# Kernel tuning notes

Measured on AMD Instinct MI355X. Metric: run time of the kernel, lower is better.

The kernel has to match this reference:

```python
import jax, jax.numpy as jnp
import numpy as np

CUT_SIZE = 224
CUTN = 128
SIDE = 1024
CUT_POW = 1.0


def setup_inputs() -> dict:
    key = jax.random.key(0)
    x = jax.random.uniform(key, (1, 3, SIDE, SIDE), dtype=jnp.float32)
    rng = np.random.default_rng(0)
    max_size = SIDE
    min_size = min(SIDE, SIDE, CUT_SIZE)
    r = rng.random(CUTN)
    sizes = (r ** CUT_POW * (max_size - min_size) + min_size).astype(np.int32)
    oy = np.array([rng.integers(0, SIDE - int(s) + 1) for s in sizes], dtype=np.int32)
    ox = np.array([rng.integers(0, SIDE - int(s) + 1) for s in sizes], dtype=np.int32)
    return {
        "input": x,
        "sizes": jnp.asarray(sizes),
        "offsety": jnp.asarray(oy),
        "offsetx": jnp.asarray(ox),
    }


def _cutout(img, size, oy, ox):
    # img: [B, C, H, W]; crop a size x size window at (oy, ox) and bilinearly
    # resample to CUT_SIZE x CUT_SIZE (align_corners=False convention).
    H, W = img.shape[2], img.shape[3]
    scale = size.astype(jnp.float32) / CUT_SIZE
    coords = (jnp.arange(CUT_SIZE, dtype=jnp.float32) + 0.5) * scale - 0.5
    ys = jnp.clip(oy.astype(jnp.float32) + coords, 0.0, H - 1.0)
    xs = jnp.clip(ox.astype(jnp.float32) + coords, 0.0, W - 1.0)
    y0 = jnp.floor(ys).astype(jnp.int32)
    x0 = jnp.floor(xs).astype(jnp.int32)
    y1 = jnp.minimum(y0 + 1, H - 1)
    x1 = jnp.minimum(x0 + 1, W - 1)
    wy = (ys - y0.astype(jnp.float32))[None, None, :, None]
    wx = (xs - x0.astype(jnp.float32))[None, None, None, :]
    # separable bilinear: interpolate rows, then columns
    rows = img[:, :, y0, :] * (1.0 - wy) + img[:, :, y1, :] * wy  # [B,C,cs,W]
    out = rows[:, :, :, x0] * (1.0 - wx) + rows[:, :, :, x1] * wx  # [B,C,cs,cs]
    return out


def _make_cutouts(input, sizes, offsety, offsetx):
    cuts = jax.vmap(_cutout, in_axes=(None, 0, 0, 0))(input, sizes, offsety, offsetx)
    # [cutn, B, C, cs, cs] -> torch.cat(dim=0) layout [cutn*B, C, cs, cs]
    n, b, c, h, w = cuts.shape
    return cuts.reshape(n * b, c, h, w)


def reference(input, sizes, offsety, offsetx):
    out = _make_cutouts(input, sizes, offsety, offsetx)
    # ClampWithGrad forward is a plain clamp
    return jnp.clip(out, 0.0, 1.0)
```

## Files before the change

### kernel.cpp

```cpp
#include <hip/hip_runtime.h>
#include <hip/hip_fp16.h>

#define CUT_SIZE 224
#define SIDE 1024
#define CUTN 128
#define NSLAB 8
#define SLAB_BLOCKS 192
#define SLAB_WSLOTS (SLAB_BLOCKS * 4)
#define LDSW2 1032

__global__ __launch_bounds__(256) void cutout_fused_kernel(
    const float* __restrict__ img,
    const int* __restrict__ sizes,
    const int* __restrict__ offy,
    const int* __restrict__ offx,
    float* __restrict__ out)
{
    __shared__ __half lds[4][3][LDSW2];
    const int s    = blockIdx.x & 7;
    const int w    = threadIdx.x >> 6;
    const int lane = threadIdx.x & 63;
    const int t    = threadIdx.x;
    const unsigned q = (unsigned)(blockIdx.x >> 3) * 4u + (unsigned)w;

    float* pf  = reinterpret_cast<float*>(&lds[0][0][0]);
    int*   pi  = reinterpret_cast<int*>(&lds[0][0][0]);
    float* fInv = pf;
    float* fOy  = pf + 128;
    int*   iWt  = pi + 256;
    int*   cdf  = pi + 384;
    int*   qbv  = pi + 513;
    int*   lenv = pi + 522;
    int*   rlov = pi + 650;
    int*   scv  = pi + 778;

    if (t < CUTN) {
        const int sz = sizes[t];
        fInv[t] = (float)CUT_SIZE / (float)sz;
        fOy[t]  = (float)offy[t];
        iWt[t]  = 100 + (sz >> 2);
    }
    __syncthreads();

    if (t <= 128) {
        const float Yf = (float)(t << 3);
        int c = 0;
        for (int n = 0; n < CUTN; ++n) {
            const float thr = (Yf + 0.5f - fOy[n]) * fInv[n] - 0.5f;
            c += min(CUT_SIZE, max(0, (int)ceilf(thr))) * iWt[n];
        }
        cdf[t] = c;
    }
    __syncthreads();

    if (t >= 1 && t < NSLAB) {
        const long long target = (long long)t * (long long)cdf[128] / NSLAB;
        int lo = 0, hi = 128;
        while (hi - lo > 1) { const int m = (lo + hi) >> 1;
                              if ((long long)cdf[m] >= target) hi = m; else lo = m; }
        qbv[t] = hi << 3;
    }
    if (t == 0) { qbv[0] = 0; qbv[NSLAB] = SIDE; }
    __syncthreads();

    if (t < CUTN) {
        int rlo, rhi;
        { const int Y = qbv[s];
          rlo = (Y <= 0) ? 0
              : min(CUT_SIZE, max(0, (int)ceilf(((float)Y + 0.5f - fOy[t]) * fInv[t] - 0.5f))); }
        { const int Y = qbv[s + 1];
          rhi = (Y >= SIDE) ? CUT_SIZE
              : min(CUT_SIZE, max(0, (int)ceilf(((float)Y + 0.5f - fOy[t]) * fInv[t] - 0.5f))); }
        rlov[t] = rlo;
        lenv[t] = rhi - rlo;
        scv[t]  = rhi - rlo;
    }
    __syncthreads();
    for (int off = 1; off < CUTN; off <<= 1) {
        int v = 0;
        if (t < CUTN && t >= off) v = scv[t - off];
        __syncthreads();
        if (t < CUTN) scv[t] += v;
        __syncthreads();
    }

    const unsigned aLo = (unsigned)(scv[lane]      - lenv[lane]);
    const unsigned aHi = (unsigned)(scv[64 + lane] - lenv[64 + lane]);
    const unsigned bLo = (unsigned)rlov[lane];
    const unsigned bHi = (unsigned)rlov[64 + lane];
    const unsigned T   = (unsigned)scv[CUTN - 1];
    const float   szLo = (float)sizes[lane], szHi = (float)sizes[64 + lane];
    const float   oyLo = (float)offy[lane],  oyHi = (float)offy[64 + lane];
    const float   oxLo = (float)offx[lane],  oxHi = (float)offx[64 + lane];
    __syncthreads();

    __half* __restrict__ l0 = &lds[w][0][0];
    __half* __restrict__ l1 = &lds[w][1][0];
    __half* __restrict__ l2 = &lds[w][2][0];

    for (unsigned i = q; i < T; i += SLAB_WSLOTS) {
        int n = 0;
        unsigned An = 0;
#pragma unroll
        for (int st = 64; st; st >>= 1) {
            const int m = n | st;
            const unsigned Am = (m & 64) ? (unsigned)__shfl((int)aHi, m & 63)
                                         : (unsigned)__shfl((int)aLo, m & 63);
            if (Am <= i) { n = m; An = Am; }
        }
        const int hi6 = n & 64, lo6 = n & 63;
        const unsigned rlo = hi6 ? (unsigned)__shfl((int)bHi, lo6)
                                 : (unsigned)__shfl((int)bLo, lo6);
        const int   y  = (int)rlo + (int)(i - An);
        const float sz = hi6 ? __shfl(szHi, lo6) : __shfl(szLo, lo6);
        const float oy = hi6 ? __shfl(oyHi, lo6) : __shfl(oyLo, lo6);
        const float ox = hi6 ? __shfl(oxHi, lo6) : __shfl(oxLo, lo6);

        const float scale = sz * (1.0f / (float)CUT_SIZE);

        float fy = fmaf((float)y + 0.5f, scale, oy - 0.5f);
        fy = fminf(fmaxf(fy, 0.0f), (float)(SIDE - 1));
        const int   y0 = (int)fy;
        const int   y1 = min(y0 + 1, SIDE - 1);
        const float wy  = fy - (float)y0;
        const float wy0 = 1.0f - wy;

        float fx0 = fmaf(0.5f, scale, ox - 0.5f);
        fx0 = fminf(fmaxf(fx0, 0.0f), (float)(SIDE - 1));
        float fxl = fmaf((float)CUT_SIZE - 0.5f, scale, ox - 0.5f);
        fxl = fminf(fmaxf(fxl, 0.0f), (float)(SIDE - 1));
        const int xb    = (int)fx0;
        const int xe    = min((int)fxl + 1, SIDE - 1);
        const int xb4   = xb & ~3;
        const int ilast = xe - xb4;
        const int nf4   = (ilast >> 2) + 1;

        const size_t cstride = (size_t)SIDE * SIDE;
        const float* b0 = img + (size_t)y0 * SIDE + xb4;
        const float* b1 = img + (size_t)y1 * SIDE + xb4;
        const float4* __restrict__ rp0 = reinterpret_cast<const float4*>(b0);
        const float4* __restrict__ rq0 = reinterpret_cast<const float4*>(b1);
        const float4* __restrict__ rp1 = reinterpret_cast<const float4*>(b0 + cstride);
        const float4* __restrict__ rq1 = reinterpret_cast<const float4*>(b1 + cstride);
        const float4* __restrict__ rp2 = reinterpret_cast<const float4*>(b0 + 2 * cstride);
        const float4* __restrict__ rq2 = reinterpret_cast<const float4*>(b1 + 2 * cstride);

        for (int k = lane; k < nf4; k += 64) {
            const float4 a0 = rp0[k], c0 = rq0[k];
            const float4 a1 = rp1[k], c1 = rq1[k];
            const float4 a2 = rp2[k], c2 = rq2[k];
            union { __half2 h[2]; uint2 u; } pk;
            pk.h[0] = __floats2half2_rn(a0.x * wy0 + c0.x * wy, a0.y * wy0 + c0.y * wy);
            pk.h[1] = __floats2half2_rn(a0.z * wy0 + c0.z * wy, a0.w * wy0 + c0.w * wy);
            *reinterpret_cast<uint2*>(l0 + 4 * k) = pk.u;
            pk.h[0] = __floats2half2_rn(a1.x * wy0 + c1.x * wy, a1.y * wy0 + c1.y * wy);
            pk.h[1] = __floats2half2_rn(a1.z * wy0 + c1.z * wy, a1.w * wy0 + c1.w * wy);
            *reinterpret_cast<uint2*>(l1 + 4 * k) = pk.u;
            pk.h[0] = __floats2half2_rn(a2.x * wy0 + c2.x * wy, a2.y * wy0 + c2.y * wy);
            pk.h[1] = __floats2half2_rn(a2.z * wy0 + c2.z * wy, a2.w * wy0 + c2.w * wy);
            *reinterpret_cast<uint2*>(l2 + 4 * k) = pk.u;
        }
        if (lane < 3) (&lds[w][lane][0])[ilast + 1] = __float2half(0.0f);
        asm volatile("s_waitcnt lgkmcnt(0)" ::: "memory");

        const int p0 = lane << 2;
        if (p0 < CUT_SIZE) {
            const float xb4f = (float)xb4;
            float fx = fmaf((float)p0 + 0.5f, scale, ox - 0.5f);
            float4 o0, o1, o2;
            float* v0 = &o0.x; float* v1 = &o1.x; float* v2 = &o2.x;
#pragma unroll
            for (int j = 0; j < 4; ++j) {
                const float fxj = fminf(fmaxf(fx, 0.0f), (float)(SIDE - 1));
                fx += scale;
                const float fl = fxj - xb4f;
                const int   i0 = (int)fl;
                const float wx  = fl - (float)i0;
                const float wx0 = 1.0f - wx;
                v0[j] = fminf(fmaxf(__half2float(l0[i0]) * wx0 + __half2float(l0[i0 + 1]) * wx, 0.0f), 1.0f);
                v1[j] = fminf(fmaxf(__half2float(l1[i0]) * wx0 + __half2float(l1[i0 + 1]) * wx, 0.0f), 1.0f);
                v2[j] = fminf(fmaxf(__half2float(l2[i0]) * wx0 + __half2float(l2[i0 + 1]) * wx, 0.0f), 1.0f);
            }
            const size_t obase = (((size_t)n * 3) * CUT_SIZE + y) * CUT_SIZE + p0;
            *reinterpret_cast<float4*>(out + obase) = o0;
            *reinterpret_cast<float4*>(out + obase + CUT_SIZE * CUT_SIZE) = o1;
            *reinterpret_cast<float4*>(out + obase + 2 * (CUT_SIZE * CUT_SIZE)) = o2;
        }
        asm volatile("" ::: "memory");
    }
}

extern "C" void kernel_launch(void* const* d_in, const int* in_sizes, int n_in,
                              void* d_out, int out_size, void* d_ws, size_t ws_size,
                              hipStream_t stream) {
    const float* img   = (const float*)d_in[0];
    const int*   sizes = (const int*)d_in[1];
    const int*   offy  = (const int*)d_in[2];
    const int*   offx  = (const int*)d_in[3];
    float*       out   = (float*)d_out;

    cutout_fused_kernel<<<NSLAB * SLAB_BLOCKS, 256, 0, stream>>>(
        img, sizes, offy, offx, out);
}
```

Baseline: 38.53 us.

## Stream source rows into LDS via global_load_lds DMA with column-chunked tasks

Replaces the per-lane float4 loads and fp16 vertical pre-interpolation with direct global-to-LDS DMA (global_load_lds, 16 bytes per lane) of fixed 256-float windows for both source rows of all three channels. Each output row is split into column chunks so the source span fits the window, and the work balancing is changed to count chunk tasks. Interpolation now runs entirely in fp32 from LDS, which also removes the half-precision rounding. The cost is more tasks with redundant window loads, scalar instead of float4 output stores, and a full vmcnt wait with no overlap between loading and compute.

```diff
diff --git a/kernel.cpp b/kernel.cpp
--- a/kernel.cpp
+++ b/kernel.cpp
@@ -1,5 +1,4 @@
 #include <hip/hip_runtime.h>
-#include <hip/hip_fp16.h>
 
 #define CUT_SIZE 224
 #define SIDE 1024
@@ -7,38 +6,50 @@
 #define NSLAB 8
 #define SLAB_BLOCKS 192
 #define SLAB_WSLOTS (SLAB_BLOCKS * 4)
-#define LDSW2 1032
-
-__global__ __launch_bounds__(256) void cutout_fused_kernel(
+#define WINF 256
+#define LWAVE (6 * WINF + 8)
+
+__device__ __forceinline__ void dma16(const float* g, float* l) {
+    __builtin_amdgcn_global_load_lds(
+        (const __attribute__((address_space(1))) void*)g,
+        (__attribute__((address_space(3))) void*)l, 16, 0, 0);
+}
+
+__global__ __launch_bounds__(256) void cutout_dma_kernel(
     const float* __restrict__ img,
     const int* __restrict__ sizes,
     const int* __restrict__ offy,
     const int* __restrict__ offx,
     float* __restrict__ out)
 {
-    __shared__ __half lds[4][3][LDSW2];
+    __shared__ float lds[4][LWAVE];
     const int s    = blockIdx.x & 7;
     const int w    = threadIdx.x >> 6;
     const int lane = threadIdx.x & 63;
     const int t    = threadIdx.x;
     const unsigned q = (unsigned)(blockIdx.x >> 3) * 4u + (unsigned)w;
 
-    float* pf  = reinterpret_cast<float*>(&lds[0][0][0]);
-    int*   pi  = reinterpret_cast<int*>(&lds[0][0][0]);
+    float* pf   = &lds[0][0];
+    int*   pi   = reinterpret_cast<int*>(&lds[0][0]);
     float* fInv = pf;
     float* fOy  = pf + 128;
-    int*   iWt  = pi + 256;
-    int*   cdf  = pi + 384;
-    int*   qbv  = pi + 513;
-    int*   lenv = pi + 522;
-    int*   rlov = pi + 650;
-    int*   scv  = pi + 778;
+    int*   iWN  = pi + 256;
+    int*   iWt  = pi + 384;
+    int*   cdf  = pi + 512;
+    int*   qbv  = pi + 641;
+    int*   lenv = pi + 650;
+    int*   rlov = pi + 778;
+    int*   scv  = pi + 906;
 
     if (t < CUTN) {
         const int sz = sizes[t];
         fInv[t] = (float)CUT_SIZE / (float)sz;
         fOy[t]  = (float)offy[t];
-        iWt[t]  = 100 + (sz >> 2);
+        int wout = 55552 / sz;
+        if (wout > CUT_SIZE) wout = CUT_SIZE;
+        const int nch = (CUT_SIZE + wout - 1) / wout;
+        iWN[t] = wout | (nch << 16);
+        iWt[t] = 8 + 5 * nch;
     }
     __syncthreads();
 
@@ -72,8 +83,9 @@
           rhi = (Y >= SIDE) ? CUT_SIZE
               : min(CUT_SIZE, max(0, (int)ceilf(((float)Y + 0.5f - fOy[t]) * fInv[t] - 0.5f))); }
         rlov[t] = rlo;
-        lenv[t] = rhi - rlo;
-        scv[t]  = rhi - rlo;
+        const int tasks = (rhi - rlo) * (iWN[t] >> 16);
+        lenv[t] = tasks;
+        scv[t]  = tasks;
     }
     __syncthreads();
     for (int off = 1; off < CUTN; off <<= 1) {
@@ -86,17 +98,16 @@
 
     const unsigned aLo = (unsigned)(scv[lane]      - lenv[lane]);
     const unsigned aHi = (unsigned)(scv[64 + lane] - lenv[64 + lane]);
-    const unsigned bLo = (unsigned)rlov[lane];
-    const unsigned bHi = (unsigned)rlov[64 + lane];
+    const unsigned rLo = (unsigned)rlov[lane],      rHi = (unsigned)rlov[64 + lane];
+    const unsigned wnLo = (unsigned)iWN[lane],      wnHi = (unsigned)iWN[64 + lane];
     const unsigned T   = (unsigned)scv[CUTN - 1];
     const float   szLo = (float)sizes[lane], szHi = (float)sizes[64 + lane];
     const float   oyLo = (float)offy[lane],  oyHi = (float)offy[64 + lane];
     const float   oxLo = (float)offx[lane],  oxHi = (float)offx[64 + lane];
     __syncthreads();
 
-    __half* __restrict__ l0 = &lds[w][0][0];
-    __half* __restrict__ l1 = &lds[w][1][0];
-    __half* __restrict__ l2 = &lds[w][2][0];
+    float* __restrict__ lw = &lds[w][0];
+    const size_t cs = (size_t)SIDE * SIDE;
 
     for (unsigned i = q; i < T; i += SLAB_WSLOTS) {
         int n = 0;
@@ -109,12 +120,21 @@
             if (Am <= i) { n = m; An = Am; }
         }
         const int hi6 = n & 64, lo6 = n & 63;
-        const unsigned rlo = hi6 ? (unsigned)__shfl((int)bHi, lo6)
-                                 : (unsigned)__shfl((int)bLo, lo6);
-        const int   y  = (int)rlo + (int)(i - An);
+        const unsigned rlo = hi6 ? (unsigned)__shfl((int)rHi, lo6)
+                                 : (unsigned)__shfl((int)rLo, lo6);
+        const unsigned wnc = hi6 ? (unsigned)__shfl((int)wnHi, lo6)
+                                 : (unsigned)__shfl((int)wnLo, lo6);
         const float sz = hi6 ? __shfl(szHi, lo6) : __shfl(szLo, lo6);
         const float oy = hi6 ? __shfl(oyHi, lo6) : __shfl(oyLo, lo6);
         const float ox = hi6 ? __shfl(oxHi, lo6) : __shfl(oxLo, lo6);
+        const int wout = (int)(wnc & 0xffffu);
+        const int nch  = (int)(wnc >> 16);
+
+        const unsigned rem = i - An;
+        const float nchinv = __builtin_amdgcn_rcpf((float)nch);
+        const int row_off = (int)(((float)rem + 0.5f) * nchinv);
+        const int chunk   = (int)rem - row_off * nch;
+        const int y       = (int)rlo + row_off;
 
         const float scale = sz * (1.0f / (float)CUT_SIZE);
 
@@ -125,66 +145,45 @@
         const float wy  = fy - (float)y0;
         const float wy0 = 1.0f - wy;
 
-        float fx0 = fmaf(0.5f, scale, ox - 0.5f);
-        fx0 = fminf(fmaxf(fx0, 0.0f), (float)(SIDE - 1));
-        float fxl = fmaf((float)CUT_SIZE - 0.5f, scale, ox - 0.5f);
-        fxl = fminf(fmaxf(fxl, 0.0f), (float)(SIDE - 1));
-        const int xb    = (int)fx0;
-        const int xe    = min((int)fxl + 1, SIDE - 1);
-        const int xb4   = xb & ~3;
-        const int ilast = xe - xb4;
-        const int nf4   = (ilast >> 2) + 1;
-
-        const size_t cstride = (size_t)SIDE * SIDE;
-        const float* b0 = img + (size_t)y0 * SIDE + xb4;
-        const float* b1 = img + (size_t)y1 * SIDE + xb4;
-        const float4* __restrict__ rp0 = reinterpret_cast<const float4*>(b0);
-        const float4* __restrict__ rq0 = reinterpret_cast<const float4*>(b1);
-        const float4* __restrict__ rp1 = reinterpret_cast<const float4*>(b0 + cstride);
-        const float4* __restrict__ rq1 = reinterpret_cast<const float4*>(b1 + cstride);
-        const float4* __restrict__ rp2 = reinterpret_cast<const float4*>(b0 + 2 * cstride);
-        const float4* __restrict__ rq2 = reinterpret_cast<const float4*>(b1 + 2 * cstride);
-
-        for (int k = lane; k < nf4; k += 64) {
-            const float4 a0 = rp0[k], c0 = rq0[k];
-            const float4 a1 = rp1[k], c1 = rq1[k];
-            const float4 a2 = rp2[k], c2 = rq2[k];
-            union { __half2 h[2]; uint2 u; } pk;
-            pk.h[0] = __floats2half2_rn(a0.x * wy0 + c0.x * wy, a0.y * wy0 + c0.y * wy);
-            pk.h[1] = __floats2half2_rn(a0.z * wy0 + c0.z * wy, a0.w * wy0 + c0.w * wy);
-            *reinterpret_cast<uint2*>(l0 + 4 * k) = pk.u;
-            pk.h[0] = __floats2half2_rn(a1.x * wy0 + c1.x * wy, a1.y * wy0 + c1.y * wy);
-            pk.h[1] = __floats2half2_rn(a1.z * wy0 + c1.z * wy, a1.w * wy0 + c1.w * wy);
-            *reinterpret_cast<uint2*>(l1 + 4 * k) = pk.u;
-            pk.h[0] = __floats2half2_rn(a2.x * wy0 + c2.x * wy, a2.y * wy0 + c2.y * wy);
-            pk.h[1] = __floats2half2_rn(a2.z * wy0 + c2.z * wy, a2.w * wy0 + c2.w * wy);
-            *reinterpret_cast<uint2*>(l2 + 4 * k) = pk.u;
-        }
-        if (lane < 3) (&lds[w][lane][0])[ilast + 1] = __float2half(0.0f);
+        const int cb   = chunk * wout;
+        const int pend = min(cb + wout, CUT_SIZE);
+
+        float fxf = fmaf((float)cb + 0.5f, scale, ox - 0.5f);
+        fxf = fminf(fmaxf(fxf, 0.0f), (float)(SIDE - 1));
+        const int xb4   = ((int)fxf) & ~3;
+        const int base2 = min(xb4, SIDE - WINF);
+
+        const float* g0 = img + (size_t)y0 * SIDE + base2 + 4 * lane;
+        const float* g1 = img + (size_t)y1 * SIDE + base2 + 4 * lane;
+
         asm volatile("s_waitcnt lgkmcnt(0)" ::: "memory");
-
-        const int p0 = lane << 2;
-        if (p0 < CUT_SIZE) {
-            const float xb4f = (float)xb4;
-            float fx = fmaf((float)p0 + 0.5f, scale, ox - 0.5f);
-            float4 o0, o1, o2;
-            float* v0 = &o0.x; float* v1 = &o1.x; float* v2 = &o2.x;
+        dma16(g0,          lw);
+        dma16(g1,          lw + WINF);
+        dma16(g0 + cs,     lw + 2 * WINF);
+        dma16(g1 + cs,     lw + 3 * WINF);
+        dma16(g0 + 2 * cs, lw + 4 * WINF);
+        dma16(g1 + 2 * cs, lw + 5 * WINF);
+        asm volatile("s_waitcnt vmcnt(0)" ::: "memory");
+
+        const size_t obase = (((size_t)n * 3) * CUT_SIZE + y) * CUT_SIZE;
+        const float b2f = (float)base2;
+
+        for (int p = cb + lane; p < pend; p += 64) {
+            float fx = fmaf((float)p + 0.5f, scale, ox - 0.5f);
+            fx = fminf(fmaxf(fx, 0.0f), (float)(SIDE - 1));
+            const float fl = fx - b2f;
+            const int   i0 = (int)fl;
+            const float wx  = fl - (float)i0;
+            const float wx0 = 1.0f - wx;
 #pragma unroll
-            for (int j = 0; j < 4; ++j) {
-                const float fxj = fminf(fmaxf(fx, 0.0f), (float)(SIDE - 1));
-                fx += scale;
-                const float fl = fxj - xb4f;
-                const int   i0 = (int)fl;
-                const float wx  = fl - (float)i0;
-                const float wx0 = 1.0f - wx;
-                v0[j] = fminf(fmaxf(__half2float(l0[i0]) * wx0 + __half2float(l0[i0 + 1]) * wx, 0.0f), 1.0f);
-                v1[j] = fminf(fmaxf(__half2float(l1[i0]) * wx0 + __half2float(l1[i0 + 1]) * wx, 0.0f), 1.0f);
-                v2[j] = fminf(fmaxf(__half2float(l2[i0]) * wx0 + __half2float(l2[i0 + 1]) * wx, 0.0f), 1.0f);
+            for (int c = 0; c < 3; ++c) {
+                const float* lc = lw + c * (2 * WINF);
+                const float a = lc[i0]     * wy0 + lc[WINF + i0]     * wy;
+                const float b = lc[i0 + 1] * wy0 + lc[WINF + i0 + 1] * wy;
+                float v = a * wx0 + b * wx;
+                v = fminf(fmaxf(v, 0.0f), 1.0f);
+                out[obase + (size_t)c * (CUT_SIZE * CUT_SIZE) + p] = v;
             }
-            const size_t obase = (((size_t)n * 3) * CUT_SIZE + y) * CUT_SIZE + p0;
-            *reinterpret_cast<float4*>(out + obase) = o0;
-            *reinterpret_cast<float4*>(out + obase + CUT_SIZE * CUT_SIZE) = o1;
-            *reinterpret_cast<float4*>(out + obase + 2 * (CUT_SIZE * CUT_SIZE)) = o2;
         }
         asm volatile("" ::: "memory");
     }
@@ -199,6 +198,6 @@
     const int*   offx  = (const int*)d_in[3];
     float*       out   = (float*)d_out;
 
-    cutout_fused_kernel<<<NSLAB * SLAB_BLOCKS, 256, 0, stream>>>(
+    cutout_dma_kernel<<<NSLAB * SLAB_BLOCKS, 256, 0, stream>>>(
         img, sizes, offy, offx, out);
 }
```

Measured after the change: 70.37 us. 1.83x slower.
